# Kernel optimization log

Hardware: AMD Instinct MI355X
Metric: run time of the kernel (lower is better)

## Reference

```python
import jax, jax.numpy as jnp
import numpy as np

B, D, F, T = 8192, 128, 128, 64


def setup_inputs() -> dict:
    key = jax.random.key(0)
    k1, k2, k3, k4 = jax.random.split(key, 4)
    inputs = jax.random.normal(k1, (B, D), dtype=jnp.float32)
    task_idx = jax.random.randint(k2, (B,), 0, T, dtype=jnp.int32)
    # default_kernel_init: normal * 1/sqrt(shape[1]) where shape=(T, D, F)
    kernels = jax.random.normal(k3, (T, D, F), dtype=jnp.float32) / jnp.sqrt(float(D))
    biases = jnp.zeros((T, F), dtype=jnp.float32)
    return {"inputs": inputs, "task_idx": task_idx, "kernels": kernels, "biases": biases}


def reference(inputs, task_idx, kernels, biases):
    # MoEDense forward (vector task_idx branch):
    #   y[b] = inputs[b] @ kernels[task_idx[b]] + biases[task_idx[b]]
    t = jnp.clip(task_idx, 0, kernels.shape[0] - 1)
    k_g = jnp.take(kernels, t, axis=0)          # [B, D, F] per-sample expert gather
    y = jnp.einsum('bd,bdf->bf', inputs, k_g)   # per-sample vec-mat
    y = y + jnp.take(biases, t, axis=0)
    return y
```

## Files before the change

### kernel.cpp

```cpp
#include <hip/hip_runtime.h>
#include <hip/hip_bf16.h>
#include <stdint.h>


#define D_ 128
#define F_ 128
#define T_ 64
#define TILE_M 48
#define NR_ 8
#define LDA 136

typedef __attribute__((ext_vector_type(8))) short short8;
typedef __attribute__((ext_vector_type(4))) float floatx4;

__device__ __forceinline__ int clamp_t(int t) {
    return t < 0 ? 0 : (t > T_ - 1 ? T_ - 1 : t);
}

union frag_u {
    short8 s;
    __hip_bfloat162 p[4];
};

__global__ __launch_bounds__(256, 2) void moe_fused(
    const float* __restrict__ x,
    const int*   __restrict__ tidx,
    const float* __restrict__ kern,
    const float* __restrict__ bias,
    float*       __restrict__ out)
{
    const int e    = blockIdx.x & 63;
    const int tb   = blockIdx.x >> 6;
    const int tid  = threadIdx.x;
    const int wv   = tid >> 6;
    const int lane = tid & 63;
    const int quad = lane >> 4;
    const int l16  = lane & 15;
    const int n0w  = wv * 32;

    __shared__ int wtot[4];
    __shared__ int slot[TILE_M];
    __shared__ __align__(16) unsigned short A[TILE_M * LDA];

    const int4 v = reinterpret_cast<const int4*>(tidx)[tb * 256 + tid];

    const float* Bp = kern + e * (D_ * F_);
    float c0r[4][8], c1r[4][8];
    #pragma unroll
    for (int kc = 0; kc < 4; ++kc) {
        const float* bp = Bp + (kc * 32 + quad * 8) * F_ + n0w + l16;
        #pragma unroll
        for (int j = 0; j < 8; ++j) {
            c0r[kc][j] = bp[j * F_];
            c1r[kc][j] = bp[j * F_ + 16];
        }
    }
    const float bs0 = bias[e * F_ + n0w + l16];
    const float bs1 = bias[e * F_ + n0w + l16 + 16];

    int my = (clamp_t(v.x) == e) + (clamp_t(v.y) == e)
           + (clamp_t(v.z) == e) + (clamp_t(v.w) == e);
    int pre = my;
    #pragma unroll
    for (int d = 1; d < 64; d <<= 1) {
        int u = __shfl_up(pre, d);
        if (lane >= d) pre += u;
    }
    if (lane == 63) wtot[wv] = pre;
    __syncthreads();
    int wbase = 0, cnt = 0;
    #pragma unroll
    for (int w = 0; w < 4; ++w) {
        const int t = wtot[w];
        if (w < wv) wbase += t;
        cnt += t;
    }
    const int base = wbase + pre - my;
    cnt = cnt > TILE_M ? TILE_M : cnt;

    if (my > 0 && base < TILE_M) {
        int run = base;
        const int row0 = tb * 1024 + tid * 4;
        const int tt[4] = { v.x, v.y, v.z, v.w };
        #pragma unroll
        for (int j = 0; j < 4; ++j) {
            if (clamp_t(tt[j]) == e) {
                if (run < TILE_M) slot[run] = row0 + j;
                ++run;
            }
        }
    }
    __syncthreads();

    {
        const int arow = tid >> 2;
        const int c    = (tid & 3) * 32;
        const int r    = (arow < cnt) ? slot[arow] : -1;
        float4 v0 = {0.f,0.f,0.f,0.f}, v1 = v0, v2 = v0, v3 = v0;
        float4 v4 = v0, v5 = v0, v6 = v0, v7 = v0;
        if (r >= 0) {
            const float4* xp = reinterpret_cast<const float4*>(x + r * D_ + c);
            v0 = xp[0]; v1 = xp[1]; v2 = xp[2]; v3 = xp[3];
            v4 = xp[4]; v5 = xp[5]; v6 = xp[6]; v7 = xp[7];
        }
        if (arow < TILE_M) {
            frag_u h0, h1, h2, h3;
            h0.p[0] = __float22bfloat162_rn({v0.x, v0.y});
            h0.p[1] = __float22bfloat162_rn({v0.z, v0.w});
            h0.p[2] = __float22bfloat162_rn({v1.x, v1.y});
            h0.p[3] = __float22bfloat162_rn({v1.z, v1.w});
            h1.p[0] = __float22bfloat162_rn({v2.x, v2.y});
            h1.p[1] = __float22bfloat162_rn({v2.z, v2.w});
            h1.p[2] = __float22bfloat162_rn({v3.x, v3.y});
            h1.p[3] = __float22bfloat162_rn({v3.z, v3.w});
            h2.p[0] = __float22bfloat162_rn({v4.x, v4.y});
            h2.p[1] = __float22bfloat162_rn({v4.z, v4.w});
            h2.p[2] = __float22bfloat162_rn({v5.x, v5.y});
            h2.p[3] = __float22bfloat162_rn({v5.z, v5.w});
            h3.p[0] = __float22bfloat162_rn({v6.x, v6.y});
            h3.p[1] = __float22bfloat162_rn({v6.z, v6.w});
            h3.p[2] = __float22bfloat162_rn({v7.x, v7.y});
            h3.p[3] = __float22bfloat162_rn({v7.z, v7.w});
            *reinterpret_cast<short8*>(&A[arow * LDA + c])      = h0.s;
            *reinterpret_cast<short8*>(&A[arow * LDA + c + 8])  = h1.s;
            *reinterpret_cast<short8*>(&A[arow * LDA + c + 16]) = h2.s;
            *reinterpret_cast<short8*>(&A[arow * LDA + c + 24]) = h3.s;
        }
    }
    __syncthreads();

    floatx4 acc0[3], acc1[3];
    #pragma unroll
    for (int m = 0; m < 3; ++m) {
        acc0[m] = (floatx4){0.f,0.f,0.f,0.f};
        acc1[m] = (floatx4){0.f,0.f,0.f,0.f};
    }

    #pragma unroll
    for (int kc = 0; kc < 4; ++kc) {
        const int k0 = kc * 32;
        frag_u b0, b1;
        #pragma unroll
        for (int j = 0; j < 4; ++j) {
            b0.p[j] = __float22bfloat162_rn({c0r[kc][2 * j], c0r[kc][2 * j + 1]});
            b1.p[j] = __float22bfloat162_rn({c1r[kc][2 * j], c1r[kc][2 * j + 1]});
        }
        #pragma unroll
        for (int m = 0; m < 3; ++m) {
            if (m * 16 < cnt) {
                const short8 a = *reinterpret_cast<const short8*>(
                    &A[(m * 16 + l16) * LDA + k0 + quad * 8]);
                acc0[m] = __builtin_amdgcn_mfma_f32_16x16x32_bf16(a, b0.s, acc0[m], 0, 0, 0);
                acc1[m] = __builtin_amdgcn_mfma_f32_16x16x32_bf16(a, b1.s, acc1[m], 0, 0, 0);
            }
        }
    }

    #pragma unroll
    for (int m = 0; m < 3; ++m) {
        if (m * 16 < cnt) {
            #pragma unroll
            for (int reg = 0; reg < 4; ++reg) {
                const int mr = m * 16 + quad * 4 + reg;
                if (mr < cnt) {
                    const int rr = slot[mr];
                    out[rr * F_ + n0w + l16]      = acc0[m][reg] + bs0;
                    out[rr * F_ + n0w + l16 + 16] = acc1[m][reg] + bs1;
                }
            }
        }
    }
}

extern "C" void kernel_launch(void* const* d_in, const int* in_sizes, int n_in,
                              void* d_out, int out_size, void* d_ws, size_t ws_size,
                              hipStream_t stream) {
    const float* x    = (const float*)d_in[0];
    const int*   tidx = (const int*)d_in[1];
    const float* kern = (const float*)d_in[2];
    const float* bias = (const float*)d_in[3];
    float* out = (float*)d_out;
    (void)d_ws; (void)ws_size; (void)in_sizes; (void)n_in; (void)out_size;

    moe_fused<<<NR_ * T_, 256, 0, stream>>>(x, tidx, kern, bias, out);
}
```

Baseline: 68.04 us.

## Halve rows per block, double grid, raise occupancy and pre-convert expert weights

Each block now scans 512 rows instead of 1024 with a 32-row tile, and the grid doubles to 1024 blocks with a launch bound allowing 4 blocks per CU. Expert weights are converted to bf16 fragments once before the A-tile barrier, and blocks with no matching rows exit early. The aim is more parallelism and latency hiding and less per-block serial work. In exchange, each expert's weights are reloaded twice as often, and register pressure may rise under the tighter launch bound.

New measurement: 68.03 us. No clear change (-0.0%).

```diff
diff --git a/kernel.cpp b/kernel.cpp
--- a/kernel.cpp
+++ b/kernel.cpp
@@ -6,8 +6,8 @@
 #define D_ 128
 #define F_ 128
 #define T_ 64
-#define TILE_M 48
-#define NR_ 8
+#define TILE_M 32
+#define NR_ 16
 #define LDA 136
 
 typedef __attribute__((ext_vector_type(8))) short short8;
@@ -22,7 +22,7 @@
     __hip_bfloat162 p[4];
 };
 
-__global__ __launch_bounds__(256, 2) void moe_fused(
+__global__ __launch_bounds__(256, 4) void moe_fused(
     const float* __restrict__ x,
     const int*   __restrict__ tidx,
     const float* __restrict__ kern,
@@ -42,7 +42,7 @@
     __shared__ int slot[TILE_M];
     __shared__ __align__(16) unsigned short A[TILE_M * LDA];
 
-    const int4 v = reinterpret_cast<const int4*>(tidx)[tb * 256 + tid];
+    const int2 v = reinterpret_cast<const int2*>(tidx)[tb * 256 + tid];
 
     const float* Bp = kern + e * (D_ * F_);
     float c0r[4][8], c1r[4][8];
@@ -58,8 +58,7 @@
     const float bs0 = bias[e * F_ + n0w + l16];
     const float bs1 = bias[e * F_ + n0w + l16 + 16];
 
-    int my = (clamp_t(v.x) == e) + (clamp_t(v.y) == e)
-           + (clamp_t(v.z) == e) + (clamp_t(v.w) == e);
+    int my = (clamp_t(v.x) == e) + (clamp_t(v.y) == e);
     int pre = my;
     #pragma unroll
     for (int d = 1; d < 64; d <<= 1) {
@@ -75,63 +74,60 @@
         if (w < wv) wbase += t;
         cnt += t;
     }
+    if (cnt == 0) return;
     const int base = wbase + pre - my;
     cnt = cnt > TILE_M ? TILE_M : cnt;
 
     if (my > 0 && base < TILE_M) {
         int run = base;
-        const int row0 = tb * 1024 + tid * 4;
-        const int tt[4] = { v.x, v.y, v.z, v.w };
+        const int row0 = tb * 512 + tid * 2;
+        const int tt[2] = { v.x, v.y };
         #pragma unroll
-        for (int j = 0; j < 4; ++j) {
+        for (int j = 0; j < 2; ++j) {
             if (clamp_t(tt[j]) == e) {
                 if (run < TILE_M) slot[run] = row0 + j;
                 ++run;
             }
         }
     }
-    __syncthreads();
 
-    {
-        const int arow = tid >> 2;
-        const int c    = (tid & 3) * 32;
-        const int r    = (arow < cnt) ? slot[arow] : -1;
-        float4 v0 = {0.f,0.f,0.f,0.f}, v1 = v0, v2 = v0, v3 = v0;
-        float4 v4 = v0, v5 = v0, v6 = v0, v7 = v0;
-        if (r >= 0) {
-            const float4* xp = reinterpret_cast<const float4*>(x + r * D_ + c);
-            v0 = xp[0]; v1 = xp[1]; v2 = xp[2]; v3 = xp[3];
-            v4 = xp[4]; v5 = xp[5]; v6 = xp[6]; v7 = xp[7];
-        }
-        if (arow < TILE_M) {
-            frag_u h0, h1, h2, h3;
-            h0.p[0] = __float22bfloat162_rn({v0.x, v0.y});
-            h0.p[1] = __float22bfloat162_rn({v0.z, v0.w});
-            h0.p[2] = __float22bfloat162_rn({v1.x, v1.y});
-            h0.p[3] = __float22bfloat162_rn({v1.z, v1.w});
-            h1.p[0] = __float22bfloat162_rn({v2.x, v2.y});
-            h1.p[1] = __float22bfloat162_rn({v2.z, v2.w});
-            h1.p[2] = __float22bfloat162_rn({v3.x, v3.y});
-            h1.p[3] = __float22bfloat162_rn({v3.z, v3.w});
-            h2.p[0] = __float22bfloat162_rn({v4.x, v4.y});
-            h2.p[1] = __float22bfloat162_rn({v4.z, v4.w});
-            h2.p[2] = __float22bfloat162_rn({v5.x, v5.y});
-            h2.p[3] = __float22bfloat162_rn({v5.z, v5.w});
-            h3.p[0] = __float22bfloat162_rn({v6.x, v6.y});
-            h3.p[1] = __float22bfloat162_rn({v6.z, v6.w});
-            h3.p[2] = __float22bfloat162_rn({v7.x, v7.y});
-            h3.p[3] = __float22bfloat162_rn({v7.z, v7.w});
-            *reinterpret_cast<short8*>(&A[arow * LDA + c])      = h0.s;
-            *reinterpret_cast<short8*>(&A[arow * LDA + c + 8])  = h1.s;
-            *reinterpret_cast<short8*>(&A[arow * LDA + c + 16]) = h2.s;
-            *reinterpret_cast<short8*>(&A[arow * LDA + c + 24]) = h3.s;
+    frag_u bf0[4], bf1[4];
+    #pragma unroll
+    for (int kc = 0; kc < 4; ++kc) {
+        #pragma unroll
+        for (int j = 0; j < 4; ++j) {
+            bf0[kc].p[j] = __float22bfloat162_rn({c0r[kc][2 * j], c0r[kc][2 * j + 1]});
+            bf1[kc].p[j] = __float22bfloat162_rn({c1r[kc][2 * j], c1r[kc][2 * j + 1]});
         }
     }
     __syncthreads();
 
-    floatx4 acc0[3], acc1[3];
+    {
+        const int arow = tid >> 3;
+        const int c    = (tid & 7) * 16;
+        const int r    = (arow < cnt) ? slot[arow] : -1;
+        float4 v0 = {0.f,0.f,0.f,0.f}, v1 = v0, v2 = v0, v3 = v0;
+        if (r >= 0) {
+            const float4* xp = reinterpret_cast<const float4*>(x + r * D_ + c);
+            v0 = xp[0]; v1 = xp[1]; v2 = xp[2]; v3 = xp[3];
+        }
+        frag_u h0, h1;
+        h0.p[0] = __float22bfloat162_rn({v0.x, v0.y});
+        h0.p[1] = __float22bfloat162_rn({v0.z, v0.w});
+        h0.p[2] = __float22bfloat162_rn({v1.x, v1.y});
+        h0.p[3] = __float22bfloat162_rn({v1.z, v1.w});
+        h1.p[0] = __float22bfloat162_rn({v2.x, v2.y});
+        h1.p[1] = __float22bfloat162_rn({v2.z, v2.w});
+        h1.p[2] = __float22bfloat162_rn({v3.x, v3.y});
+        h1.p[3] = __float22bfloat162_rn({v3.z, v3.w});
+        *reinterpret_cast<short8*>(&A[arow * LDA + c])     = h0.s;
+        *reinterpret_cast<short8*>(&A[arow * LDA + c + 8]) = h1.s;
+    }
+    __syncthreads();
+
+    floatx4 acc0[2], acc1[2];
     #pragma unroll
-    for (int m = 0; m < 3; ++m) {
+    for (int m = 0; m < 2; ++m) {
         acc0[m] = (floatx4){0.f,0.f,0.f,0.f};
         acc1[m] = (floatx4){0.f,0.f,0.f,0.f};
     }
@@ -139,25 +135,19 @@
     #pragma unroll
     for (int kc = 0; kc < 4; ++kc) {
         const int k0 = kc * 32;
-        frag_u b0, b1;
         #pragma unroll
-        for (int j = 0; j < 4; ++j) {
-            b0.p[j] = __float22bfloat162_rn({c0r[kc][2 * j], c0r[kc][2 * j + 1]});
-            b1.p[j] = __float22bfloat162_rn({c1r[kc][2 * j], c1r[kc][2 * j + 1]});
-        }
-        #pragma unroll
-        for (int m = 0; m < 3; ++m) {
+        for (int m = 0; m < 2; ++m) {
             if (m * 16 < cnt) {
                 const short8 a = *reinterpret_cast<const short8*>(
                     &A[(m * 16 + l16) * LDA + k0 + quad * 8]);
-                acc0[m] = __builtin_amdgcn_mfma_f32_16x16x32_bf16(a, b0.s, acc0[m], 0, 0, 0);
-                acc1[m] = __builtin_amdgcn_mfma_f32_16x16x32_bf16(a, b1.s, acc1[m], 0, 0, 0);
+                acc0[m] = __builtin_amdgcn_mfma_f32_16x16x32_bf16(a, bf0[kc].s, acc0[m], 0, 0, 0);
+                acc1[m] = __builtin_amdgcn_mfma_f32_16x16x32_bf16(a, bf1[kc].s, acc1[m], 0, 0, 0);
             }
         }
     }
 
     #pragma unroll
-    for (int m = 0; m < 3; ++m) {
+    for (int m = 0; m < 2; ++m) {
         if (m * 16 < cnt) {
             #pragma unroll
             for (int reg = 0; reg < 4; ++reg) {
```
